# Performance work log

Hardware: AMD Instinct MI355X
Metric: run time of the kernel (lower is better)

## Reference

```python
import jax, jax.numpy as jnp
import numpy as np

N_HEADS = 16


def setup_inputs() -> dict:
    key = jax.random.key(0)
    k1, k2 = jax.random.split(key)
    B, S, D = 2, 2048, 2048
    x = jax.random.normal(k1, (B, S, D), dtype=jnp.float32)
    # torch nn.Linear(dim, 3*dim): y = x @ W^T + b; store W in jax layout [D, 3D]
    W_qkv = jax.random.normal(k2, (D, 3 * D), dtype=jnp.float32) * (D ** -0.5)
    b_qkv = jnp.zeros((3 * D,), dtype=jnp.float32)
    mask = jnp.ones((B, S), dtype=bool)
    return {"x": x, "W_qkv": W_qkv, "b_qkv": b_qkv, "mask": mask}


def reference(x, W_qkv, b_qkv, mask):
    B, S, D = x.shape
    H = N_HEADS
    hd = D // H
    scale = hd ** -0.5
    qkv = x @ W_qkv + b_qkv                      # [B,S,3D]
    q, k, v = jnp.split(qkv, 3, axis=-1)
    # [B,S,D] -> [B,H,S,hd]
    reshape = lambda t: t.reshape(B, S, H, hd).transpose(0, 2, 1, 3)
    q, k, v = reshape(q), reshape(k), reshape(v)
    sim = jnp.einsum('bhqd,bhkd->bhqk', q, k) * scale   # [B,H,S,S]
    neg = -jnp.finfo(sim.dtype).max
    sim = jnp.where(mask[:, None, None, :], sim, neg)   # padding mask on keys
    attn = jax.nn.softmax(sim, axis=-1)
    out = jnp.einsum('bhqk,bhkd->bhqd', attn, v)        # [B,H,S,hd]
    return out.transpose(0, 2, 1, 3).reshape(B, S, D)
```

## Files before the change

### kernel.cpp

```cpp
#include <hip/hip_runtime.h>
#include <hip/hip_bf16.h>
#include <math.h>

typedef __attribute__((ext_vector_type(8))) short bf16x8;
typedef __attribute__((ext_vector_type(4))) float f32x4;
typedef __attribute__((ext_vector_type(16))) float f32x16;
typedef __attribute__((ext_vector_type(4))) short short4v;
typedef __attribute__((ext_vector_type(4))) int int4v;

__device__ __forceinline__ short f2bf(float f) {
  union { float f; unsigned u; } v; v.f = f;
  unsigned r = v.u + 0x7fffu + ((v.u >> 16) & 1u);
  return (short)(r >> 16);
}

__device__ __forceinline__ unsigned cvt_pk_bf16(float lo, float hi) {
  unsigned r;
  asm volatile("v_cvt_pk_bf16_f32 %0, %1, %2" : "=v"(r) : "v"(lo), "v"(hi));
  return r;
}


__global__ void convert_x_kernel(const float* __restrict__ x, short* __restrict__ xb, int n) {
  int i = (blockIdx.x * blockDim.x + threadIdx.x) * 4;
  int stride = gridDim.x * blockDim.x * 4;
  for (; i < n; i += stride) {
    float4 v = *(const float4*)(x + i);
    short4v o;
    o.x = f2bf(v.x); o.y = f2bf(v.y); o.z = f2bf(v.z); o.w = f2bf(v.w);
    *(short4v*)(xb + i) = o;
  }
}

__global__ void transpose_w_kernel(const float* __restrict__ W, short* __restrict__ Wt) {
  __shared__ short tile[32][33];
  int n0 = blockIdx.x * 32, k0 = blockIdx.y * 32;
  int tx = threadIdx.x, ty = threadIdx.y;
#pragma unroll
  for (int u = 0; u < 4; ++u) {
    int k = k0 + ty + u * 8;
    tile[ty + u * 8][tx] = f2bf(W[(size_t)k * 6144 + n0 + tx]);
  }
  __syncthreads();
#pragma unroll
  for (int u = 0; u < 4; ++u) {
    int n = n0 + ty + u * 8;
    Wt[(size_t)n * 2048 + k0 + tx] = tile[tx][ty + u * 8];
  }
}

__global__ void mask_norm_kernel(const unsigned* __restrict__ m, unsigned char* __restrict__ out, int n) {
  __shared__ int flagA, flagB;
  if (threadIdx.x == 0) { flagA = 0; flagB = 0; }
  __syncthreads();
  int a = 0, b = 0;
  for (int i = threadIdx.x; i < n / 4; i += blockDim.x) {
    unsigned wv = m[i];
    if (wv > 1u) a = 1;
    if (wv != 0u && wv != 0x3f800000u) b = 1;
  }
  if (a) atomicOr(&flagA, 1);
  if (b) atomicOr(&flagB, 1);
  __syncthreads();
  int A = flagA, B = flagB;
  for (int i = threadIdx.x; i < n; i += blockDim.x) {
    unsigned char r;
    if (!A) r = (m[i] != 0u) ? 1 : 0;
    else if (!B) r = (((const float*)m)[i] != 0.f) ? 1 : 0;
    else r = (((const unsigned char*)m)[i] != 0) ? 1 : 0;
    out[i] = r;
  }
}


__global__ __launch_bounds__(512, 2) void qkv_gemm_kernel(
    const short* __restrict__ A, const short* __restrict__ Bt, const float* __restrict__ bias,
    short* __restrict__ qws, short* __restrict__ kws, short* __restrict__ vtws) {
  __shared__ __align__(16) char smem[131072];

  int lid = blockIdx.x;
  int swz = (lid & 7) * 48 + (lid >> 3);
  int tm = swz / 24, tn = swz % 24;
  int m0 = tm * 256, n0 = tn * 256;
  int t = threadIdx.x, lane = t & 63, w = t >> 6;
  int wr = w >> 2, wc = w & 3;
  int g = lane >> 4, c = lane & 15;

#define AHP(P, hm) (smem + (P) * 65536 + (hm) * 16384)
#define BHP(P, hn) (smem + (P) * 65536 + 32768 + (hn) * 16384)

#define STAGE_HALF(ldsb, gbase)                                                            \
  { _Pragma("unroll")                                                                      \
    for (int rr = 0; rr < 2; ++rr) {                                                       \
      int ci = rr * 512 + t;                                                               \
      int row_ = ci >> 3, ch_ = ci & 7;                                                    \
      const short* gp_ = (gbase) + (size_t)row_ * 2048 + ((ch_ ^ (row_ & 7)) * 8);         \
      __builtin_amdgcn_global_load_lds((const __attribute__((address_space(1))) void*)gp_, \
          (__attribute__((address_space(3))) void*)((ldsb) + ci * 16), 16, 0, 0);          \
    } }

#define LD_A(half)                                                                          \
  { const char* ab_ = AHP(P, half);                                                         \
    _Pragma("unroll")                                                                       \
    for (int mi = 0; mi < 4; ++mi) {                                                        \
      int row_ = wr * 16 + c + mi * 32;                                                     \
      _Pragma("unroll")                                                                     \
      for (int ks = 0; ks < 2; ++ks)                                                        \
        af[mi][ks] = *(const bf16x8*)(ab_ + row_ * 128 + (((ks * 4 + g) ^ (row_ & 7)) * 16)); \
    } }
#define LD_B(half)                                                                          \
  { const char* bb_ = BHP(P, half);                                                         \
    _Pragma("unroll")                                                                       \
    for (int nj = 0; nj < 2; ++nj) {                                                        \
      int row_ = wc * 16 + c + nj * 64;                                                     \
      _Pragma("unroll")                                                                     \
      for (int ks = 0; ks < 2; ++ks)                                                        \
        bfr[nj][ks] = *(const bf16x8*)(bb_ + row_ * 128 + (((ks * 4 + g) ^ (row_ & 7)) * 16)); \
    } }
#define MFMA16(MI0, NJ0)                                                                    \
  __builtin_amdgcn_s_setprio(1);                                                            \
  _Pragma("unroll")                                                                         \
  for (int mi = 0; mi < 4; ++mi)                                                            \
    _Pragma("unroll")                                                                       \
    for (int nj = 0; nj < 2; ++nj)                                                          \
      _Pragma("unroll")                                                                     \
      for (int ks = 0; ks < 2; ++ks)                                                        \
        acc[(MI0) + mi][(NJ0) + nj] =                                                       \
            __builtin_amdgcn_mfma_f32_16x16x32_bf16(af[mi][ks], bfr[nj][ks],                \
                                                    acc[(MI0) + mi][(NJ0) + nj], 0, 0, 0);  \
  __builtin_amdgcn_s_setprio(0);

  STAGE_HALF(AHP(0, 0), A + (size_t)m0 * 2048);
  STAGE_HALF(BHP(0, 0), Bt + (size_t)n0 * 2048);
  STAGE_HALF(BHP(0, 1), Bt + (size_t)(n0 + 128) * 2048);
  STAGE_HALF(AHP(0, 1), A + (size_t)(m0 + 128) * 2048);
  asm volatile("s_waitcnt vmcnt(4)" ::: "memory");
  __builtin_amdgcn_s_barrier();

  f32x4 acc[8][4] = {};

  for (int tk = 0; tk < 32; ++tk) {
    int P = tk & 1, Pn = P ^ 1;
    bool pf = (tk + 1 < 32);
    int k1 = (tk + 1) * 64;
    bf16x8 af[4][2], bfr[2][2];

    LD_A(0); LD_B(0);
    if (pf) STAGE_HALF(AHP(Pn, 0), A + (size_t)m0 * 2048 + k1);
    MFMA16(0, 0);
    if (pf) { asm volatile("s_waitcnt vmcnt(4)" ::: "memory"); }
    else    { asm volatile("s_waitcnt vmcnt(2)" ::: "memory"); }
    __builtin_amdgcn_s_barrier();

    LD_B(1);
    if (pf) STAGE_HALF(BHP(Pn, 0), Bt + (size_t)n0 * 2048 + k1);
    MFMA16(0, 2);
    if (pf) { asm volatile("s_waitcnt vmcnt(4)" ::: "memory"); }
    else    { asm volatile("s_waitcnt vmcnt(0)" ::: "memory"); }
    __builtin_amdgcn_s_barrier();

    LD_A(1);
    if (pf) STAGE_HALF(BHP(Pn, 1), Bt + (size_t)(n0 + 128) * 2048 + k1);
    MFMA16(4, 2);
    __builtin_amdgcn_s_barrier();

    LD_B(0);
    if (pf) STAGE_HALF(AHP(Pn, 1), A + (size_t)(m0 + 128) * 2048 + k1);
    MFMA16(4, 0);
    if (pf) { asm volatile("s_waitcnt vmcnt(4)" ::: "memory"); }
    __builtin_amdgcn_s_barrier();
  }

  int sec = n0 >> 11;
  int b = m0 >> 11;
  int s0 = m0 & 2047;
  int nsec = n0 & 2047;

  if (sec < 2) {
    short* base = (sec == 0 ? qws : kws);
    const float scq = (sec == 0) ? (0.08838834764831845f * 1.4426950408889634f) : 1.0f;
#pragma unroll
    for (int nj = 0; nj < 4; ++nj) {
      int colsec = nsec + wc * 16 + nj * 64;
      float bv = bias[n0 + wc * 16 + nj * 64 + c];
      int h = colsec >> 7;
      int d = (colsec & 127) + c;
      short* dst = base + ((size_t)(b * 16 + h)) * (2048 * 128) + d;
#pragma unroll
      for (int mi = 0; mi < 8; ++mi) {
        int srow = s0 + (wr + 2 * mi) * 16 + g * 4;
#pragma unroll
        for (int r = 0; r < 4; ++r)
          dst[(size_t)(srow + r) * 128] = f2bf((acc[mi][nj][r] + bv) * scq);
      }
    }
  } else {
    __builtin_amdgcn_s_barrier();
    char* wreg = smem + w * 16384;
#pragma unroll
    for (int nj = 0; nj < 4; ++nj) {
      float bv = bias[n0 + wc * 16 + nj * 64 + c];
      int d = nj * 16 + c;
#pragma unroll
      for (int mi = 0; mi < 8; ++mi)
#pragma unroll
        for (int r = 0; r < 4; ++r) {
          int sloc = mi * 16 + g * 4 + r;
          *(short*)(wreg + d * 256 + (((sloc >> 3) ^ (d & 15)) * 16) + (sloc & 7) * 2) =
              f2bf(acc[mi][nj][r] + bv);
        }
    }
#pragma unroll
    for (int q = 0; q < 16; ++q) {
      int d = q * 4 + g;
      bf16x8 v = *(const bf16x8*)(wreg + d * 256 + ((c ^ (d & 15)) * 16));
      int colsec = nsec + wc * 16 + (d >> 4) * 64 + (d & 15);
      int h = colsec >> 7, dloc = colsec & 127;
      int srow = s0 + wr * 16 + (c >> 1) * 32 + (c & 1) * 8;
      *(bf16x8*)(vtws + ((size_t)(b * 16 + h)) * (128 * 2048) + (size_t)dloc * 2048 + srow) = v;
    }
  }
#undef AHP
#undef BHP
#undef STAGE_HALF
#undef LD_A
#undef LD_B
#undef MFMA16
}


__global__ __launch_bounds__(256, 2) void attn_kernel(
    const short* __restrict__ qws, const short* __restrict__ kws, const short* __restrict__ vtws,
    const unsigned char* __restrict__ maskb, float* __restrict__ out) {
  __shared__ short Ks[2][32 * 128];
  __shared__ short Vs[2][128 * 32];
  __shared__ short P[4][32 * 40];
  __shared__ float biasLds[2048];
  __shared__ int flagsLds[64];

  const int S = 2048, HD = 128;
  int lid = blockIdx.x;
  int swz = (lid & 7) * 64 + (lid >> 3);
  int bh = swz >> 4, qblk = swz & 15;
  int b = bh >> 4, h = bh & 15;
  int t = threadIdx.x, lane = t & 63, w = t >> 6;
  int ql = lane & 31, hi = lane >> 5;
  int q0 = qblk * 128 + w * 32;
  const short* Q = qws + (size_t)bh * S * HD;
  const short* Kp = kws + (size_t)bh * S * HD;
  const short* Vt = vtws + (size_t)bh * HD * S;
  const unsigned char* mk = maskb + b * S;
  const float NEG = -3.4028235e38f;

#define STAGE_KV(buf, kv0_)                                                              \
  {                                                                                      \
    _Pragma("unroll")                                                                    \
    for (int rr = 0; rr < 2; ++rr) {                                                     \
      int ci = rr * 256 + t;                                                             \
      int r = ci >> 4, cin = ci & 15;                                                    \
      const short* gk = Kp + (size_t)((kv0_) + r) * HD + ((cin ^ (r & 7)) * 8);          \
      __builtin_amdgcn_global_load_lds((const __attribute__((address_space(1))) void*)gk,\
          (__attribute__((address_space(3))) void*)(&Ks[buf][0] + ci * 8), 16, 0, 0);    \
    }                                                                                    \
    _Pragma("unroll")                                                                    \
    for (int rr = 0; rr < 2; ++rr) {                                                     \
      int ci = rr * 256 + t;                                                             \
      int r = ci >> 2, cin = ci & 3;                                                     \
      const short* gv = Vt + (size_t)r * S + (kv0_) + ((cin ^ ((r >> 1) & 3)) * 8);      \
      __builtin_amdgcn_global_load_lds((const __attribute__((address_space(1))) void*)gv,\
          (__attribute__((address_space(3))) void*)(&Vs[buf][0] + ci * 8), 16, 0, 0);    \
    }                                                                                    \
  }

  bf16x8 qf[8];
#pragma unroll
  for (int kc = 0; kc < 8; ++kc)
    qf[kc] = *(const bf16x8*)(Q + (size_t)(q0 + ql) * HD + kc * 16 + hi * 8);

  for (int i = t; i < 2048; i += 256) biasLds[i] = mk[i] ? 0.f : NEG;
  STAGE_KV(0, 0);
  __syncthreads();
  if (t < 64) {
    int ok = 1;
    for (int j = 0; j < 32; ++j) ok &= (biasLds[t * 32 + j] == 0.f) ? 1 : 0;
    flagsLds[t] = ok;
  }
  __syncthreads();

  f32x16 acc[4] = {};
  float m_ = NEG, lp = 0.f;
  short* pl = &P[w][0];
  int cur = 0;

  for (int it = 0; it < 64; ++it) {
    int kv0 = it * 32;
    if (it + 1 < 64) STAGE_KV(cur ^ 1, kv0 + 32);

    const short* ks = &Ks[cur][0];
    const short* vs = &Vs[cur][0];

    f32x16 sv = {};
    __builtin_amdgcn_s_setprio(1);
#pragma unroll
    for (int kc = 0; kc < 8; ++kc) {
      int chunk = (kc * 2 + hi) ^ (ql & 7);
      bf16x8 kf = *(const bf16x8*)(ks + ql * 128 + chunk * 8);
      sv = __builtin_amdgcn_mfma_f32_32x32x16_bf16(kf, qf[kc], sv, 0, 0, 0);
    }
    __builtin_amdgcn_s_setprio(0);

    float p[16];
    int fl = flagsLds[it];
    if (fl) {
#pragma unroll
      for (int r = 0; r < 16; ++r) p[r] = sv[r];
    } else {
#pragma unroll
      for (int g2 = 0; g2 < 4; ++g2) {
        f32x4 bb = *(const f32x4*)(biasLds + kv0 + g2 * 8 + hi * 4);
#pragma unroll
        for (int j = 0; j < 4; ++j) p[g2 * 4 + j] = sv[g2 * 4 + j] + bb[j];
      }
    }

    float a0 = fmaxf(fmaxf(p[0], p[1]), fmaxf(p[2], p[3]));
    float a1 = fmaxf(fmaxf(p[4], p[5]), fmaxf(p[6], p[7]));
    float a2 = fmaxf(fmaxf(p[8], p[9]), fmaxf(p[10], p[11]));
    float a3 = fmaxf(fmaxf(p[12], p[13]), fmaxf(p[14], p[15]));
    float rmx = fmaxf(fmaxf(a0, a1), fmaxf(a2, a3));
    rmx = fmaxf(rmx, __shfl_xor(rmx, 32));

    if (__any(rmx > m_ + 12.f)) {
      float mn = fmaxf(m_, rmx);
      float al = exp2f(m_ - mn);
      m_ = mn; lp *= al;
#pragma unroll
      for (int dt = 0; dt < 4; ++dt)
#pragma unroll
        for (int r = 0; r < 16; ++r) acc[dt][r] *= al;
    }

    float e[16];
#pragma unroll
    for (int r = 0; r < 16; ++r) e[r] = exp2f(p[r] - m_);
    float s0 = ((e[0] + e[1]) + (e[2] + e[3])) + ((e[4] + e[5]) + (e[6] + e[7]));
    float s1 = ((e[8] + e[9]) + (e[10] + e[11])) + ((e[12] + e[13]) + (e[14] + e[15]));
    lp += s0 + s1;

#pragma unroll
    for (int g2 = 0; g2 < 4; ++g2) {
      int2 pk;
      pk.x = (int)cvt_pk_bf16(e[4 * g2 + 0], e[4 * g2 + 1]);
      pk.y = (int)cvt_pk_bf16(e[4 * g2 + 2], e[4 * g2 + 3]);
      *(int2*)(pl + ql * 40 + g2 * 8 + hi * 4) = pk;
    }

    bf16x8 pf[2];
#pragma unroll
    for (int kt = 0; kt < 2; ++kt)
      pf[kt] = *(const bf16x8*)(pl + ql * 40 + (kt * 2 + hi) * 8);

    __builtin_amdgcn_s_setprio(1);
#pragma unroll
    for (int dt = 0; dt < 4; ++dt) {
      int d = dt * 32 + ql;
#pragma unroll
      for (int kt = 0; kt < 2; ++kt) {
        int chunk = (kt * 2 + hi) ^ ((d >> 1) & 3);
        bf16x8 vf = *(const bf16x8*)(vs + d * 32 + chunk * 8);
        acc[dt] = __builtin_amdgcn_mfma_f32_32x32x16_bf16(vf, pf[kt], acc[dt], 0, 0, 0);
      }
    }
    __builtin_amdgcn_s_setprio(0);

    __syncthreads();
    cur ^= 1;
  }

  lp += __shfl_xor(lp, 32);
  float inv = 1.f / lp;
  size_t orow = (size_t)(b * 2048 + q0 + ql) * 2048 + h * 128;
#pragma unroll
  for (int dt = 0; dt < 4; ++dt)
#pragma unroll
    for (int g2 = 0; g2 < 4; ++g2) {
      f32x4 v;
      v[0] = acc[dt][g2 * 4 + 0] * inv;
      v[1] = acc[dt][g2 * 4 + 1] * inv;
      v[2] = acc[dt][g2 * 4 + 2] * inv;
      v[3] = acc[dt][g2 * 4 + 3] * inv;
      int d = dt * 32 + g2 * 8 + hi * 4;
      *(f32x4*)(out + orow + d) = v;
    }
#undef STAGE_KV
}


extern "C" void kernel_launch(void* const* d_in, const int* in_sizes, int n_in,
                              void* d_out, int out_size, void* d_ws, size_t ws_size,
                              hipStream_t stream) {
  const float* x = (const float*)d_in[0];
  const float* W = (const float*)d_in[1];
  const float* bias = (const float*)d_in[2];
  const void* mask = d_in[3];
  float* out = (float*)d_out;

  char* ws = (char*)d_ws;
  short* xb = (short*)(ws);
  short* wt = (short*)(ws + 16777216);
  short* qws = (short*)(ws + 41943040);
  short* kws = (short*)(ws + 58720256);
  short* vtws = (short*)(ws + 75497472);
  unsigned char* maskb = (unsigned char*)(ws + 92274688);

  convert_x_kernel<<<dim3(2048), dim3(256), 0, stream>>>(x, xb, 2 * 2048 * 2048);
  transpose_w_kernel<<<dim3(192, 64), dim3(32, 8), 0, stream>>>(W, wt);
  mask_norm_kernel<<<dim3(1), dim3(256), 0, stream>>>((const unsigned*)mask, maskb, 2 * 2048);
  qkv_gemm_kernel<<<dim3(384), dim3(512), 0, stream>>>(xb, wt, bias, qws, kws, vtws);
  attn_kernel<<<dim3(512), dim3(256), 0, stream>>>(qws, kws, vtws, maskb, out);
}
```

Measured before the change: 350.0 us.

## Software-pipeline attention loop so PV overlaps next tile's softmax, via register permlane

Restructures the attention main loop so the QK MFMAs for tile i run alongside the PV MFMAs for tile i-1, while softmax for tile i runs afterwards. V fragments are preloaded into registers before the buffer is overwritten. The P tile no longer makes a round trip through LDS: packed bf16 probabilities are rearranged between lanes with v_permlane32_swap. Per-tile mask flags move into a wave-level ballot bitmask instead of an LDS read every iteration. The cost is extra register pressure from the vreg and pfv fragments held across the loop, plus a more complicated prologue and epilogue.

```diff
diff --git a/kernel.cpp b/kernel.cpp
--- a/kernel.cpp
+++ b/kernel.cpp
@@ -7,6 +7,7 @@
 typedef __attribute__((ext_vector_type(16))) float f32x16;
 typedef __attribute__((ext_vector_type(4))) short short4v;
 typedef __attribute__((ext_vector_type(4))) int int4v;
+typedef __attribute__((ext_vector_type(4))) unsigned uint4v;
 
 __device__ __forceinline__ short f2bf(float f) {
   union { float f; unsigned u; } v; v.f = f;
@@ -234,7 +235,6 @@
     const unsigned char* __restrict__ maskb, float* __restrict__ out) {
   __shared__ short Ks[2][32 * 128];
   __shared__ short Vs[2][128 * 32];
-  __shared__ short P[4][32 * 40];
   __shared__ float biasLds[2048];
   __shared__ int flagsLds[64];
 
@@ -272,6 +272,73 @@
     }                                                                                    \
   }
 
+#define QK_PHASE(CUR)                                                                    \
+  { const short* ks = &Ks[CUR][0];                                                       \
+    _Pragma("unroll") for (int r = 0; r < 16; ++r) sv[r] = 0.f;                          \
+    __builtin_amdgcn_s_setprio(1);                                                       \
+    _Pragma("unroll") for (int kc = 0; kc < 8; ++kc) {                                   \
+      int chunk = (kc * 2 + hi) ^ (ql & 7);                                              \
+      bf16x8 kf = *(const bf16x8*)(ks + ql * 128 + chunk * 8);                           \
+      sv = __builtin_amdgcn_mfma_f32_32x32x16_bf16(kf, qf[kc], sv, 0, 0, 0);             \
+    }                                                                                    \
+    __builtin_amdgcn_s_setprio(0); }
+
+#define PV_PHASE()                                                                       \
+  { __builtin_amdgcn_s_setprio(1);                                                       \
+    _Pragma("unroll") for (int dt = 0; dt < 4; ++dt)                                     \
+      _Pragma("unroll") for (int kt = 0; kt < 2; ++kt)                                   \
+        acc[dt] = __builtin_amdgcn_mfma_f32_32x32x16_bf16(vreg[dt * 2 + kt], pfv[kt],    \
+                                                          acc[dt], 0, 0, 0);             \
+    __builtin_amdgcn_s_setprio(0); }
+
+#define LOADV(CUR)                                                                       \
+  { const short* vs = &Vs[CUR][0];                                                       \
+    _Pragma("unroll") for (int dt = 0; dt < 4; ++dt)                                     \
+      _Pragma("unroll") for (int kt = 0; kt < 2; ++kt) {                                 \
+        int d = dt * 32 + ql;                                                            \
+        int chunk = (kt * 2 + hi) ^ ((d >> 1) & 3);                                      \
+        vreg[dt * 2 + kt] = *(const bf16x8*)(vs + d * 32 + chunk * 8);                   \
+      } }
+
+#define SOFTMAX_PACK(IT_)                                                                \
+  { int kv0s = (IT_) * 32;                                                               \
+    float p[16];                                                                         \
+    if ((fmask >> (IT_)) & 1ull) {                                                       \
+      _Pragma("unroll") for (int r = 0; r < 16; ++r) p[r] = sv[r];                       \
+    } else {                                                                             \
+      _Pragma("unroll") for (int g2 = 0; g2 < 4; ++g2) {                                 \
+        f32x4 bb = *(const f32x4*)(biasLds + kv0s + g2 * 8 + hi * 4);                    \
+        _Pragma("unroll") for (int j = 0; j < 4; ++j)                                    \
+          p[g2 * 4 + j] = sv[g2 * 4 + j] + bb[j];                                        \
+      }                                                                                  \
+    }                                                                                    \
+    float a0 = fmaxf(fmaxf(p[0], p[1]), fmaxf(p[2], p[3]));                              \
+    float a1 = fmaxf(fmaxf(p[4], p[5]), fmaxf(p[6], p[7]));                              \
+    float a2 = fmaxf(fmaxf(p[8], p[9]), fmaxf(p[10], p[11]));                            \
+    float a3 = fmaxf(fmaxf(p[12], p[13]), fmaxf(p[14], p[15]));                          \
+    float rmx = fmaxf(fmaxf(a0, a1), fmaxf(a2, a3));                                     \
+    rmx = fmaxf(rmx, __shfl_xor(rmx, 32));                                               \
+    if (__any(rmx > m_ + 12.f)) {                                                        \
+      float mn = fmaxf(m_, rmx);                                                         \
+      float al = exp2f(m_ - mn);                                                         \
+      m_ = mn; lp *= al;                                                                 \
+      _Pragma("unroll") for (int dt = 0; dt < 4; ++dt)                                   \
+        _Pragma("unroll") for (int r = 0; r < 16; ++r) acc[dt][r] *= al;                 \
+    }                                                                                    \
+    _Pragma("unroll") for (int r = 0; r < 16; ++r) p[r] = exp2f(p[r] - m_);              \
+    lp += (((p[0] + p[1]) + (p[2] + p[3])) + ((p[4] + p[5]) + (p[6] + p[7])))            \
+        + (((p[8] + p[9]) + (p[10] + p[11])) + ((p[12] + p[13]) + (p[14] + p[15])));     \
+    _Pragma("unroll") for (int kt = 0; kt < 2; ++kt) {                                   \
+      unsigned Aw = cvt_pk_bf16(p[kt * 8 + 0], p[kt * 8 + 1]);                           \
+      unsigned Bw = cvt_pk_bf16(p[kt * 8 + 2], p[kt * 8 + 3]);                           \
+      unsigned Cw = cvt_pk_bf16(p[kt * 8 + 4], p[kt * 8 + 5]);                           \
+      unsigned Dw = cvt_pk_bf16(p[kt * 8 + 6], p[kt * 8 + 7]);                           \
+      asm volatile("v_permlane32_swap_b32 %0, %1" : "+v"(Aw), "+v"(Cw));                 \
+      asm volatile("v_permlane32_swap_b32 %0, %1" : "+v"(Bw), "+v"(Dw));                 \
+      uint4v uu; uu.x = Aw; uu.y = Bw; uu.z = Cw; uu.w = Dw;                             \
+      pfv[kt] = __builtin_bit_cast(bf16x8, uu);                                          \
+    } }
+
   bf16x8 qf[8];
 #pragma unroll
   for (int kc = 0; kc < 8; ++kc)
@@ -286,96 +353,30 @@
     flagsLds[t] = ok;
   }
   __syncthreads();
+  unsigned long long fmask = __ballot(flagsLds[lane] != 0);
 
   f32x16 acc[4] = {};
   float m_ = NEG, lp = 0.f;
-  short* pl = &P[w][0];
-  int cur = 0;
-
-  for (int it = 0; it < 64; ++it) {
-    int kv0 = it * 32;
-    if (it + 1 < 64) STAGE_KV(cur ^ 1, kv0 + 32);
-
-    const short* ks = &Ks[cur][0];
-    const short* vs = &Vs[cur][0];
-
-    f32x16 sv = {};
-    __builtin_amdgcn_s_setprio(1);
-#pragma unroll
-    for (int kc = 0; kc < 8; ++kc) {
-      int chunk = (kc * 2 + hi) ^ (ql & 7);
-      bf16x8 kf = *(const bf16x8*)(ks + ql * 128 + chunk * 8);
-      sv = __builtin_amdgcn_mfma_f32_32x32x16_bf16(kf, qf[kc], sv, 0, 0, 0);
-    }
-    __builtin_amdgcn_s_setprio(0);
-
-    float p[16];
-    int fl = flagsLds[it];
-    if (fl) {
-#pragma unroll
-      for (int r = 0; r < 16; ++r) p[r] = sv[r];
-    } else {
-#pragma unroll
-      for (int g2 = 0; g2 < 4; ++g2) {
-        f32x4 bb = *(const f32x4*)(biasLds + kv0 + g2 * 8 + hi * 4);
-#pragma unroll
-        for (int j = 0; j < 4; ++j) p[g2 * 4 + j] = sv[g2 * 4 + j] + bb[j];
-      }
-    }
-
-    float a0 = fmaxf(fmaxf(p[0], p[1]), fmaxf(p[2], p[3]));
-    float a1 = fmaxf(fmaxf(p[4], p[5]), fmaxf(p[6], p[7]));
-    float a2 = fmaxf(fmaxf(p[8], p[9]), fmaxf(p[10], p[11]));
-    float a3 = fmaxf(fmaxf(p[12], p[13]), fmaxf(p[14], p[15]));
-    float rmx = fmaxf(fmaxf(a0, a1), fmaxf(a2, a3));
-    rmx = fmaxf(rmx, __shfl_xor(rmx, 32));
-
-    if (__any(rmx > m_ + 12.f)) {
-      float mn = fmaxf(m_, rmx);
-      float al = exp2f(m_ - mn);
-      m_ = mn; lp *= al;
-#pragma unroll
-      for (int dt = 0; dt < 4; ++dt)
-#pragma unroll
-        for (int r = 0; r < 16; ++r) acc[dt][r] *= al;
-    }
-
-    float e[16];
-#pragma unroll
-    for (int r = 0; r < 16; ++r) e[r] = exp2f(p[r] - m_);
-    float s0 = ((e[0] + e[1]) + (e[2] + e[3])) + ((e[4] + e[5]) + (e[6] + e[7]));
-    float s1 = ((e[8] + e[9]) + (e[10] + e[11])) + ((e[12] + e[13]) + (e[14] + e[15]));
-    lp += s0 + s1;
-
-#pragma unroll
-    for (int g2 = 0; g2 < 4; ++g2) {
-      int2 pk;
-      pk.x = (int)cvt_pk_bf16(e[4 * g2 + 0], e[4 * g2 + 1]);
-      pk.y = (int)cvt_pk_bf16(e[4 * g2 + 2], e[4 * g2 + 3]);
-      *(int2*)(pl + ql * 40 + g2 * 8 + hi * 4) = pk;
-    }
-
-    bf16x8 pf[2];
-#pragma unroll
-    for (int kt = 0; kt < 2; ++kt)
-      pf[kt] = *(const bf16x8*)(pl + ql * 40 + (kt * 2 + hi) * 8);
-
-    __builtin_amdgcn_s_setprio(1);
-#pragma unroll
-    for (int dt = 0; dt < 4; ++dt) {
-      int d = dt * 32 + ql;
-#pragma unroll
-      for (int kt = 0; kt < 2; ++kt) {
-        int chunk = (kt * 2 + hi) ^ ((d >> 1) & 3);
-        bf16x8 vf = *(const bf16x8*)(vs + d * 32 + chunk * 8);
-        acc[dt] = __builtin_amdgcn_mfma_f32_32x32x16_bf16(vf, pf[kt], acc[dt], 0, 0, 0);
-      }
-    }
-    __builtin_amdgcn_s_setprio(0);
-
+  f32x16 sv;
+  bf16x8 pfv[2];
+  bf16x8 vreg[8];
+
+  QK_PHASE(0);
+  STAGE_KV(1, 32);
+  SOFTMAX_PACK(0);
+  LOADV(0);
+  __syncthreads();
+
+  for (int it = 1; it < 64; ++it) {
+    int cur = it & 1;
+    QK_PHASE(cur);
+    if (it < 63) STAGE_KV(cur ^ 1, it * 32 + 32);
+    PV_PHASE();
+    LOADV(cur);
+    SOFTMAX_PACK(it);
     __syncthreads();
-    cur ^= 1;
-  }
+  }
+  PV_PHASE();
 
   lp += __shfl_xor(lp, 32);
   float inv = 1.f / lp;
@@ -393,6 +394,10 @@
       *(f32x4*)(out + orow + d) = v;
     }
 #undef STAGE_KV
+#undef QK_PHASE
+#undef PV_PHASE
+#undef LOADV
+#undef SOFTMAX_PACK
 }
 
 
```

Result: faster. 334.9 us (-4.3%).
